# Kernel tuning notes

Measured on AMD Instinct MI355X. Metric: run time of the kernel, lower is better.

## Reference

```python
import jax, jax.numpy as jnp
import numpy as np

B, S, E, H, D = 2, 2048, 1024, 16, 64  # batch, seq(=max_seq_len), embed_dim, heads, atten_dim


def setup_inputs() -> dict:
    key = jax.random.key(0)
    ks = jax.random.split(key, 9)
    s = 0.02
    return {
        "x": jax.random.normal(ks[0], (B, S, E), jnp.float32),
        "Wq": jax.random.normal(ks[1], (H, E, D), jnp.float32) * s,
        "Wk": jax.random.normal(ks[2], (H, E, D), jnp.float32) * s,
        "Wv": jax.random.normal(ks[3], (H, E, D), jnp.float32) * s,
        "bq": jax.random.normal(ks[4], (H, D), jnp.float32) * s,
        "bk": jax.random.normal(ks[5], (H, D), jnp.float32) * s,
        "bv": jax.random.normal(ks[6], (H, D), jnp.float32) * s,
        "Wp": jax.random.normal(ks[7], (H * D, E), jnp.float32) * s,
        "bp": jax.random.normal(ks[8], (E,), jnp.float32) * s,
    }


def reference(x, Wq, Wk, Wv, bq, bk, bv, Wp, bp):
    scale = jnp.sqrt(jnp.float32(D))
    # per-head projections, all heads at once: [B,H,S,D]
    q = jnp.einsum("bse,hed->bhsd", x, Wq) + bq[:, None, :]
    k = jnp.einsum("bse,hed->bhsd", x, Wk) + bk[:, None, :]
    v = jnp.einsum("bse,hed->bhsd", x, Wv) + bv[:, None, :]
    # causal scores [B,H,S,S], additive -inf mask above diagonal (as in the buffer)
    score = jnp.einsum("bhsd,bhtd->bhst", q, k) / scale
    mask = jnp.triu(jnp.full((S, S), -jnp.inf, jnp.float32), k=1)
    score = score + mask
    probs = jax.nn.softmax(score, axis=-1)
    attn = jnp.einsum("bhst,bhtd->bhsd", probs, v)
    # concat heads -> [B,S,H*D], then projection + ReLU
    concat = attn.transpose(0, 2, 1, 3).reshape(B, S, H * D)
    out = jax.nn.relu(concat @ Wp + bp)
    return out
```

## Files before the change

### kernel.cpp

```cpp
#include <hip/hip_runtime.h>

#define S_LEN 2048
#define E_DIM 1024
#define H_NUM 16
#define D_DIM 64

typedef unsigned short u16;
using bf16x8 = __attribute__((ext_vector_type(8))) short;
using f32x4  = __attribute__((ext_vector_type(4))) float;

#define MFMA16(A, B, C) __builtin_amdgcn_mfma_f32_16x16x32_bf16(A, B, C, 0, 0, 0)
#define QSCALE 0.18033688011112042f

__device__ __forceinline__ u16 f2bf(float f) {
    unsigned u = __float_as_uint(f);
    u += 0x7fffu + ((u >> 16) & 1u);
    return (u16)(u >> 16);
}
__device__ __forceinline__ f32x4 fzero4() { f32x4 z; z[0]=0.f; z[1]=0.f; z[2]=0.f; z[3]=0.f; return z; }

__device__ __forceinline__ unsigned cvtpk(float a, float b) {
    unsigned r;
    asm("v_cvt_pk_bf16_f32 %0, %1, %2" : "=v"(r) : "v"(a), "v"(b));
    return r;
}
__device__ __forceinline__ float fexp2(float x) {
#if __has_builtin(__builtin_amdgcn_exp2f)
    return __builtin_amdgcn_exp2f(x);
#else
    float r; asm("v_exp_f32 %0, %1" : "=v"(r) : "v"(x)); return r;
#endif
}
__device__ __forceinline__ float frcp(float x) {
#if __has_builtin(__builtin_amdgcn_rcpf)
    return __builtin_amdgcn_rcpf(x);
#else
    float r; asm("v_rcp_f32 %0, %1" : "=v"(r) : "v"(x)); return r;
#endif
}

__device__ __forceinline__ void gll16(const u16* g, u16* l) {
    __builtin_amdgcn_global_load_lds(
        (const __attribute__((address_space(1))) void*)g,
        (__attribute__((address_space(3))) void*)l, 16, 0, 0);
}

__device__ __forceinline__ void stage64(const u16* __restrict__ g, int gstride,
                                        u16* l, int wave, int lane) {
    #pragma unroll
    for (int i = 0; i < 2; i++) {
        const int r  = wave * 16 + i * 8 + (lane >> 3);
        const int sl = (lane & 7) ^ (r & 7);
        gll16(g + (size_t)r * gstride + sl * 8, l + (wave * 16 + i * 8) * 64);
    }
}
__device__ __forceinline__ bf16x8 ldswz(const u16* t, int rr, int hh, int quad) {
    const int sl = ((hh << 2) + quad) ^ (rr & 7);
    return *(const bf16x8*)(t + rr * 64 + sl * 8);
}

__global__ __launch_bounds__(256) void cvt_bf16(const float* __restrict__ in, u16* __restrict__ outp, int n) {
    int i4 = (blockIdx.x * 256 + threadIdx.x) * 4;
    if (i4 < n) {
        float4 f = *(const float4*)(in + i4);
        unsigned lo = (unsigned)f2bf(f.x) | ((unsigned)f2bf(f.y) << 16);
        unsigned hi = (unsigned)f2bf(f.z) | ((unsigned)f2bf(f.w) << 16);
        uint2 p; p.x = lo; p.y = hi;
        *(uint2*)(outp + i4) = p;
    }
}

__device__ __forceinline__ void cvt_t_tile(const float* __restrict__ bin, u16* __restrict__ bout,
                                           int R, int C, int r0, int c0) {
    __shared__ float t[64][65];
    const int tid = threadIdx.x;
    const int lr = tid >> 2, lc = (tid & 3) * 16;

    const float* src = bin + (size_t)(r0 + lr) * C + c0 + lc;
    #pragma unroll
    for (int j = 0; j < 4; j++) {
        float4 f = *(const float4*)(src + j * 4);
        t[lr][lc + j * 4 + 0] = f.x; t[lr][lc + j * 4 + 1] = f.y;
        t[lr][lc + j * 4 + 2] = f.z; t[lr][lc + j * 4 + 3] = f.w;
    }
    __syncthreads();

    u16* dst = bout + (size_t)(c0 + lr) * R + r0 + lc;
    u16 vals[16];
    #pragma unroll
    for (int i = 0; i < 16; i++) vals[i] = f2bf(t[lc + i][lr]);
    uint4 pa, pb;
    pa.x = vals[0] | (vals[1] << 16);  pa.y = vals[2] | (vals[3] << 16);
    pa.z = vals[4] | (vals[5] << 16);  pa.w = vals[6] | (vals[7] << 16);
    pb.x = vals[8] | (vals[9] << 16);  pb.y = vals[10] | (vals[11] << 16);
    pb.z = vals[12] | (vals[13] << 16); pb.w = vals[14] | (vals[15] << 16);
    *(uint4*)dst = pa;
    *(uint4*)(dst + 8) = pb;
}

__global__ __launch_bounds__(256) void cvt_bf16_t(const float* __restrict__ in, u16* __restrict__ outp,
                                                  int R, int C) {
    const float* bin = in + (size_t)blockIdx.z * R * C;
    u16* bout = outp + (size_t)blockIdx.z * R * C;
    cvt_t_tile(bin, bout, R, C, blockIdx.y * 64, blockIdx.x * 64);
}

__global__ __launch_bounds__(256) void cvt_w3_t(
    const float* __restrict__ Wq, const float* __restrict__ Wk, const float* __restrict__ Wv,
    u16* __restrict__ wqt, u16* __restrict__ wkt, u16* __restrict__ wvt) {
    const int which = blockIdx.z >> 4, bh = blockIdx.z & 15;
    const float* in = (which == 0) ? Wq : (which == 1) ? Wk : Wv;
    u16* outp = (which == 0) ? wqt : (which == 1) ? wkt : wvt;
    const float* bin = in + (size_t)bh * E_DIM * D_DIM;
    u16* bout = outp + (size_t)bh * E_DIM * D_DIM;
    cvt_t_tile(bin, bout, E_DIM, D_DIM, blockIdx.y * 64, 0);
}

__global__ __launch_bounds__(256) void qkv_gemm(
    const u16* __restrict__ xb, const u16* __restrict__ wcat,
    const float* __restrict__ bq, const float* __restrict__ bk, const float* __restrict__ bv,
    u16* __restrict__ oq, u16* __restrict__ okk, u16* __restrict__ ov)
{
    const int m0 = blockIdx.x * 128;
    const int n0 = blockIdx.y * 128;

    __shared__ u16 As[128 * 64];
    __shared__ u16 Bs[128 * 64];

    const int tid  = threadIdx.x;
    const int wave = tid >> 6, lane = tid & 63, quad = lane >> 4, l16 = lane & 15;
    const int mh = wave >> 1, nh = wave & 1;

    f32x4 acc[4][4];
    #pragma unroll
    for (int j = 0; j < 4; j++)
        #pragma unroll
        for (int mi = 0; mi < 4; mi++) acc[j][mi] = fzero4();

    for (int k0 = 0; k0 < E_DIM; k0 += 64) {
        __syncthreads();
        #pragma unroll
        for (int i = 0; i < 4; i++) {
            const int r  = wave * 32 + i * 8 + (lane >> 3);
            const int sl = (lane & 7) ^ (r & 7);
            gll16(xb   + (size_t)(m0 + r) * E_DIM + k0 + sl * 8, &As[(wave * 32 + i * 8) * 64]);
            gll16(wcat + (size_t)(n0 + r) * E_DIM + k0 + sl * 8, &Bs[(wave * 32 + i * 8) * 64]);
        }
        __syncthreads();

        #pragma unroll
        for (int kq = 0; kq < 2; kq++) {
            bf16x8 af[4];
            #pragma unroll
            for (int mi = 0; mi < 4; mi++) {
                const int rr = mh * 64 + mi * 16 + l16;
                af[mi] = *(const bf16x8*)(&As[rr * 64 + (((kq << 2) + quad) ^ (rr & 7)) * 8]);
            }
            #pragma unroll
            for (int j = 0; j < 4; j++) {
                const int rr = nh * 64 + j * 16 + l16;
                bf16x8 bfv = *(const bf16x8*)(&Bs[rr * 64 + (((kq << 2) + quad) ^ (rr & 7)) * 8]);
                #pragma unroll
                for (int mi = 0; mi < 4; mi++)
                    acc[j][mi] = MFMA16(af[mi], bfv, acc[j][mi]);
            }
        }
    }

    const int t = n0 >> 10;
    if (t < 2) {
        const float scl = (t == 0) ? QSCALE : 1.0f;
        const float* bias = (t == 0) ? bq : bk;
        u16* dst = (t == 0) ? oq : okk;
        #pragma unroll
        for (int j = 0; j < 4; j++) {
            const int n = n0 + nh * 64 + j * 16 + l16;
            const int h = (n >> 6) & 15, d = n & 63;
            float bia = bias[h * D_DIM + d];
            #pragma unroll
            for (int mi = 0; mi < 4; mi++) {
                #pragma unroll
                for (int r = 0; r < 4; r++) {
                    int m = m0 + mh * 64 + mi * 16 + quad * 4 + r;
                    int b = m >> 11, s = m & 2047;
                    dst[((size_t)(b * H_NUM + h) * S_LEN + s) * D_DIM + d] =
                        f2bf((acc[j][mi][r] + bia) * scl);
                }
            }
        }
    } else {
        const int b  = m0 >> 11, s0 = m0 & 2047;
        const int h0 = (n0 >> 6) & 15;
        u16* Tb0 = As;
        u16* Tb1 = Bs;
        #pragma unroll
        for (int pass = 0; pass < 2; ++pass) {
            __syncthreads();
            if (mh == pass) {
                u16* Tb = nh ? Tb1 : Tb0;
                #pragma unroll
                for (int j = 0; j < 4; j++) {
                    const int n = n0 + nh * 64 + j * 16 + l16;
                    const int d = n & 63, hh = (n >> 6) & 15;
                    const float bia = bv[hh * D_DIM + d];
                    const int nl = j * 16 + l16;
                    #pragma unroll
                    for (int mi = 0; mi < 4; mi++) {
                        uint2 pk;
                        pk.x = cvtpk(acc[j][mi][0] + bia, acc[j][mi][1] + bia);
                        pk.y = cvtpk(acc[j][mi][2] + bia, acc[j][mi][3] + bia);
                        *(uint2*)(&Tb[nl * 72 + mi * 16 + quad * 4]) = pk;
                    }
                }
            }
            __syncthreads();
            #pragma unroll
            for (int g = 0; g < 4; ++g) {
                const int rowi = g * 32 + (tid >> 3);
                const int ml = (tid & 7) * 8;
                const u16* srcp = (rowi < 64 ? Tb0 : Tb1) + (rowi & 63) * 72 + ml;
                const int hh = h0 + (rowi >> 6), d = rowi & 63;
                u16* dstp = ov + ((size_t)(b * H_NUM + hh) * D_DIM + d) * S_LEN
                               + s0 + pass * 64 + ml;
                *(uint4*)dstp = *(const uint4*)srcp;
            }
        }
    }
}

__global__ __launch_bounds__(256, 2) void attn_fwd(
    const u16* __restrict__ q, const u16* __restrict__ k, const u16* __restrict__ vt,
    u16* __restrict__ concat)
{
    const int bid  = blockIdx.x;
    const int halfg = bid >> 8;
    const int pi   = (bid & 255) >> 5;
    const int p    = halfg ? (15 - pi) : pi;
    const int g    = bid & 31;
    const int h    = g & 15;
    const int bb   = g >> 4;
    const int qa = p, qb = 31 - p;

    const size_t headoff = (size_t)(bb * H_NUM + h) * S_LEN * D_DIM;
    const u16* qh  = q  + headoff;
    const u16* kh  = k  + headoff;
    const u16* vth = vt + headoff;

    __shared__ u16 QaL[64 * 64];
    __shared__ u16 QbL[64 * 64];
    __shared__ u16 Ks[2][64 * 64];
    __shared__ u16 Vts[2][64 * 64];
    __shared__ u16 Psa[4][16 * 72];
    __shared__ u16 Psb[4][16 * 72];

    const int tid  = threadIdx.x;
    const int wave = tid >> 6, lane = tid & 63, quad = lane >> 4, l16 = lane & 15;

    stage64(qh + (size_t)qa * 64 * D_DIM, D_DIM, QaL,    wave, lane);
    stage64(qh + (size_t)qb * 64 * D_DIM, D_DIM, QbL,    wave, lane);
    stage64(kh,                           D_DIM, Ks[0],  wave, lane);
    stage64(vth,                          S_LEN, Vts[0], wave, lane);
    __syncthreads();

    bf16x8 bqa0 = ldswz(QaL, wave * 16 + l16, 0, quad);
    bf16x8 bqa1 = ldswz(QaL, wave * 16 + l16, 1, quad);
    bf16x8 bqb0 = ldswz(QbL, wave * 16 + l16, 0, quad);
    bf16x8 bqb1 = ldswz(QbL, wave * 16 + l16, 1, quad);

    f32x4 oa[4], ob[4];
    #pragma unroll
    for (int nt = 0; nt < 4; nt++) { oa[nt] = fzero4(); ob[nt] = fzero4(); }
    float la = 0.f, lb = 0.f;

    const int qga = qa * 64 + wave * 16 + l16;
    const int qgb = qb * 64 + wave * 16 + l16;

    u16* pwa = &Psa[wave][0];
    u16* pwb = &Psb[wave][0];

    for (int kt = 0; kt <= qb; kt++) {
        __syncthreads();
        if (kt < qb) {
            stage64(kh + (size_t)(kt + 1) * 64 * D_DIM, D_DIM, Ks[(kt + 1) & 1],  wave, lane);
            stage64(vth + (kt + 1) * 64,                S_LEN, Vts[(kt + 1) & 1], wave, lane);
        }
        const u16* Kc = Ks[kt & 1];
        const u16* Vc = Vts[kt & 1];
        const bool both = (kt <= qa);

        f32x4 stb[4], sta[4];
        #pragma unroll
        for (int nt = 0; nt < 4; nt++) {
            const int rr = nt * 16 + l16;
            bf16x8 ak0 = ldswz(Kc, rr, 0, quad);
            bf16x8 ak1 = ldswz(Kc, rr, 1, quad);
            stb[nt] = MFMA16(ak0, bqb0, fzero4());
            stb[nt] = MFMA16(ak1, bqb1, stb[nt]);
            if (both) {
                sta[nt] = MFMA16(ak0, bqa0, fzero4());
                sta[nt] = MFMA16(ak1, bqa1, sta[nt]);
            }
        }

        bf16x8 bv0[4], bv1[4];
        #pragma unroll
        for (int nt = 0; nt < 4; nt++) {
            bv0[nt] = ldswz(Vc, nt * 16 + l16, 0, quad);
            bv1[nt] = ldswz(Vc, nt * 16 + l16, 1, quad);
        }

        #pragma unroll
        for (int nt = 0; nt < 4; nt++) {
            float pe[4];
            if (kt == qb) {
                #pragma unroll
                for (int r = 0; r < 4; r++) {
                    int kkg = kt * 64 + nt * 16 + quad * 4 + r;
                    pe[r] = (kkg > qgb) ? 0.f : fexp2(stb[nt][r]);
                }
            } else {
                #pragma unroll
                for (int r = 0; r < 4; r++) pe[r] = fexp2(stb[nt][r]);
            }
            lb += (pe[0] + pe[1]) + (pe[2] + pe[3]);
            uint2 pk;
            pk.x = cvtpk(pe[0], pe[1]);
            pk.y = cvtpk(pe[2], pe[3]);
            *(uint2*)(&pwb[l16 * 72 + nt * 16 + quad * 4]) = pk;
        }
        if (both) {
            #pragma unroll
            for (int nt = 0; nt < 4; nt++) {
                float pe[4];
                if (kt == qa) {
                    #pragma unroll
                    for (int r = 0; r < 4; r++) {
                        int kkg = kt * 64 + nt * 16 + quad * 4 + r;
                        pe[r] = (kkg > qga) ? 0.f : fexp2(sta[nt][r]);
                    }
                } else {
                    #pragma unroll
                    for (int r = 0; r < 4; r++) pe[r] = fexp2(sta[nt][r]);
                }
                la += (pe[0] + pe[1]) + (pe[2] + pe[3]);
                uint2 pk;
                pk.x = cvtpk(pe[0], pe[1]);
                pk.y = cvtpk(pe[2], pe[3]);
                *(uint2*)(&pwa[l16 * 72 + nt * 16 + quad * 4]) = pk;
            }
        }

        {
            bf16x8 ap0 = *(const bf16x8*)(&pwb[l16 * 72 + quad * 8]);
            bf16x8 ap1 = *(const bf16x8*)(&pwb[l16 * 72 + 32 + quad * 8]);
            #pragma unroll
            for (int nt = 0; nt < 4; nt++) {
                ob[nt] = MFMA16(ap0, bv0[nt], ob[nt]);
                ob[nt] = MFMA16(ap1, bv1[nt], ob[nt]);
            }
        }
        if (both) {
            bf16x8 ap0 = *(const bf16x8*)(&pwa[l16 * 72 + quad * 8]);
            bf16x8 ap1 = *(const bf16x8*)(&pwa[l16 * 72 + 32 + quad * 8]);
            #pragma unroll
            for (int nt = 0; nt < 4; nt++) {
                oa[nt] = MFMA16(ap0, bv0[nt], oa[nt]);
                oa[nt] = MFMA16(ap1, bv1[nt], oa[nt]);
            }
        }
    }

    lb += __shfl_xor(lb, 16); lb += __shfl_xor(lb, 32);
    la += __shfl_xor(la, 16); la += __shfl_xor(la, 32);

    #pragma unroll
    for (int r = 0; r < 4; r++) {
        const int srcl = quad * 4 + r;
        float lbi = frcp(__shfl(lb, srcl));
        float lai = frcp(__shfl(la, srcl));
        int sqa = qa * 64 + wave * 16 + quad * 4 + r;
        int sqb = qb * 64 + wave * 16 + quad * 4 + r;
        #pragma unroll
        for (int nt = 0; nt < 4; nt++) {
            concat[((size_t)(bb * S_LEN + sqa)) * E_DIM + h * D_DIM + nt * 16 + l16] =
                f2bf(oa[nt][r] * lai);
            concat[((size_t)(bb * S_LEN + sqb)) * E_DIM + h * D_DIM + nt * 16 + l16] =
                f2bf(ob[nt][r] * lbi);
        }
    }
}

__global__ __launch_bounds__(256) void out_proj(
    const u16* __restrict__ concat, const u16* __restrict__ wpt,
    const float* __restrict__ bp, float* __restrict__ out)
{
    const int m0 = blockIdx.x * 128;
    const int n0 = blockIdx.y * 128;

    __shared__ u16 As[128 * 40];
    __shared__ u16 Bs[128 * 40];

    const int tid  = threadIdx.x;
    const int wave = tid >> 6, lane = tid & 63, quad = lane >> 4, l16 = lane & 15;
    const int mh = wave >> 1, nh = wave & 1;

    const int arow = tid >> 1, acol = (tid & 1) * 16;

    const u16* aptr = concat + (size_t)(m0 + arow) * E_DIM + acol;
    const u16* bptr = wpt + (size_t)(n0 + arow) * E_DIM + acol;

    f32x4 acc[4][4];
    #pragma unroll
    for (int j = 0; j < 4; j++)
        #pragma unroll
        for (int mi = 0; mi < 4; mi++) acc[j][mi] = fzero4();

    uint4 pA0, pA1, pB0, pB1;
    pA0 = *(const uint4*)(aptr);     pA1 = *(const uint4*)(aptr + 8);
    pB0 = *(const uint4*)(bptr);     pB1 = *(const uint4*)(bptr + 8);

    for (int k0 = 0; k0 < E_DIM; k0 += 32) {
        __syncthreads();
        *(uint4*)(&As[arow * 40 + acol    ]) = pA0;
        *(uint4*)(&As[arow * 40 + acol + 8]) = pA1;
        *(uint4*)(&Bs[arow * 40 + acol    ]) = pB0;
        *(uint4*)(&Bs[arow * 40 + acol + 8]) = pB1;
        __syncthreads();

        if (k0 + 32 < E_DIM) {
            pA0 = *(const uint4*)(aptr + k0 + 32);  pA1 = *(const uint4*)(aptr + k0 + 40);
            pB0 = *(const uint4*)(bptr + k0 + 32);  pB1 = *(const uint4*)(bptr + k0 + 40);
        }

        bf16x8 af[4];
        #pragma unroll
        for (int mi = 0; mi < 4; mi++)
            af[mi] = *(const bf16x8*)(&As[(mh * 64 + mi * 16 + l16) * 40 + quad * 8]);
        #pragma unroll
        for (int j = 0; j < 4; j++) {
            bf16x8 bfv = *(const bf16x8*)(&Bs[(nh * 64 + j * 16 + l16) * 40 + quad * 8]);
            #pragma unroll
            for (int mi = 0; mi < 4; mi++)
                acc[j][mi] = MFMA16(af[mi], bfv, acc[j][mi]);
        }
    }

    #pragma unroll
    for (int j = 0; j < 4; j++) {
        int n = n0 + nh * 64 + j * 16 + l16;
        float bia = bp[n];
        #pragma unroll
        for (int mi = 0; mi < 4; mi++) {
            #pragma unroll
            for (int r = 0; r < 4; r++) {
                int m = m0 + mh * 64 + mi * 16 + quad * 4 + r;
                out[(size_t)m * E_DIM + n] = fmaxf(acc[j][mi][r] + bia, 0.f);
            }
        }
    }
}

extern "C" void kernel_launch(void* const* d_in, const int* in_sizes, int n_in,
                              void* d_out, int out_size, void* d_ws, size_t ws_size,
                              hipStream_t stream)
{
    (void)in_sizes; (void)n_in; (void)out_size; (void)ws_size;
    const float* x  = (const float*)d_in[0];
    const float* Wq = (const float*)d_in[1];
    const float* Wk = (const float*)d_in[2];
    const float* Wv = (const float*)d_in[3];
    const float* bq = (const float*)d_in[4];
    const float* bk = (const float*)d_in[5];
    const float* bv = (const float*)d_in[6];
    const float* Wp = (const float*)d_in[7];
    const float* bp = (const float*)d_in[8];
    float* out = (float*)d_out;

    const size_t QKV_ELEMS = (size_t)2 * H_NUM * S_LEN * D_DIM;
    const size_t W_ELEMS   = (size_t)H_NUM * E_DIM * D_DIM;

    u16* q   = (u16*)d_ws;
    u16* k   = q   + QKV_ELEMS;
    u16* v   = k   + QKV_ELEMS;
    u16* cc  = v   + QKV_ELEMS;
    u16* xb  = cc  + QKV_ELEMS;
    u16* wqt = xb  + QKV_ELEMS;
    u16* wkt = wqt + W_ELEMS;
    u16* wvt = wkt + W_ELEMS;
    u16* wpt = wvt + W_ELEMS;

    cvt_bf16<<<dim3(4096), 256, 0, stream>>>(x, xb, (int)QKV_ELEMS);
    cvt_w3_t<<<dim3(1, 16, 48), 256, 0, stream>>>(Wq, Wk, Wv, wqt, wkt, wvt);
    cvt_bf16_t<<<dim3(16, 16, 1), 256, 0, stream>>>(Wp, wpt, H_NUM * D_DIM, E_DIM);

    qkv_gemm<<<dim3(32, 24), 256, 0, stream>>>(xb, wqt, bq, bk, bv, q, k, v);
    attn_fwd<<<dim3(512), 256, 0, stream>>>(q, k, v, cc);
    out_proj<<<dim3(32, 8), 256, 0, stream>>>(cc, wpt, bp, out);
}
```

Before: 191.7 us.

## Merge conversion kernels, swizzle GEMM block order, and retile out_proj with LDS DMA

New measurement: 182.9 us. 4.6% less time.

```diff
diff --git a/kernel.cpp b/kernel.cpp
--- a/kernel.cpp
+++ b/kernel.cpp
@@ -57,17 +57,6 @@
 __device__ __forceinline__ bf16x8 ldswz(const u16* t, int rr, int hh, int quad) {
     const int sl = ((hh << 2) + quad) ^ (rr & 7);
     return *(const bf16x8*)(t + rr * 64 + sl * 8);
-}
-
-__global__ __launch_bounds__(256) void cvt_bf16(const float* __restrict__ in, u16* __restrict__ outp, int n) {
-    int i4 = (blockIdx.x * 256 + threadIdx.x) * 4;
-    if (i4 < n) {
-        float4 f = *(const float4*)(in + i4);
-        unsigned lo = (unsigned)f2bf(f.x) | ((unsigned)f2bf(f.y) << 16);
-        unsigned hi = (unsigned)f2bf(f.z) | ((unsigned)f2bf(f.w) << 16);
-        uint2 p; p.x = lo; p.y = hi;
-        *(uint2*)(outp + i4) = p;
-    }
 }
 
 __device__ __forceinline__ void cvt_t_tile(const float* __restrict__ bin, u16* __restrict__ bout,
@@ -98,22 +87,35 @@
     *(uint4*)(dst + 8) = pb;
 }
 
-__global__ __launch_bounds__(256) void cvt_bf16_t(const float* __restrict__ in, u16* __restrict__ outp,
-                                                  int R, int C) {
-    const float* bin = in + (size_t)blockIdx.z * R * C;
-    u16* bout = outp + (size_t)blockIdx.z * R * C;
-    cvt_t_tile(bin, bout, R, C, blockIdx.y * 64, blockIdx.x * 64);
-}
-
-__global__ __launch_bounds__(256) void cvt_w3_t(
+__global__ __launch_bounds__(256) void cvt_all(
+    const float* __restrict__ x, u16* __restrict__ xb, int n,
     const float* __restrict__ Wq, const float* __restrict__ Wk, const float* __restrict__ Wv,
-    u16* __restrict__ wqt, u16* __restrict__ wkt, u16* __restrict__ wvt) {
-    const int which = blockIdx.z >> 4, bh = blockIdx.z & 15;
-    const float* in = (which == 0) ? Wq : (which == 1) ? Wk : Wv;
-    u16* outp = (which == 0) ? wqt : (which == 1) ? wkt : wvt;
-    const float* bin = in + (size_t)bh * E_DIM * D_DIM;
-    u16* bout = outp + (size_t)bh * E_DIM * D_DIM;
-    cvt_t_tile(bin, bout, E_DIM, D_DIM, blockIdx.y * 64, 0);
+    u16* __restrict__ wqt, u16* __restrict__ wkt, u16* __restrict__ wvt,
+    const float* __restrict__ Wp, u16* __restrict__ wpt)
+{
+    const int bid = blockIdx.x;
+    if (bid < 4096) {
+        int i4 = (bid * 256 + threadIdx.x) * 4;
+        if (i4 < n) {
+            float4 f = *(const float4*)(x + i4);
+            unsigned lo = (unsigned)f2bf(f.x) | ((unsigned)f2bf(f.y) << 16);
+            unsigned hi = (unsigned)f2bf(f.z) | ((unsigned)f2bf(f.w) << 16);
+            uint2 p; p.x = lo; p.y = hi;
+            *(uint2*)(xb + i4) = p;
+        }
+    } else if (bid < 4096 + 768) {
+        const int t  = bid - 4096;
+        const int z  = t >> 4;
+        const int ry = t & 15;
+        const int which = z >> 4, bh = z & 15;
+        const float* in = (which == 0) ? Wq : (which == 1) ? Wk : Wv;
+        u16* outp = (which == 0) ? wqt : (which == 1) ? wkt : wvt;
+        cvt_t_tile(in + (size_t)bh * E_DIM * D_DIM, outp + (size_t)bh * E_DIM * D_DIM,
+                   E_DIM, D_DIM, ry * 64, 0);
+    } else {
+        const int t = bid - (4096 + 768);
+        cvt_t_tile(Wp, wpt, H_NUM * D_DIM, E_DIM, (t >> 4) * 64, (t & 15) * 64);
+    }
 }
 
 __global__ __launch_bounds__(256) void qkv_gemm(
@@ -121,8 +123,10 @@
     const float* __restrict__ bq, const float* __restrict__ bk, const float* __restrict__ bv,
     u16* __restrict__ oq, u16* __restrict__ okk, u16* __restrict__ ov)
 {
-    const int m0 = blockIdx.x * 128;
-    const int n0 = blockIdx.y * 128;
+    const int bid = blockIdx.x;
+    const int sw  = (bid & 7) * 96 + (bid >> 3);
+    const int m0  = (sw & 31) * 128;
+    const int n0  = (sw >> 5) * 128;
 
     __shared__ u16 As[128 * 64];
     __shared__ u16 Bs[128 * 64];
@@ -289,6 +293,7 @@
         const bool both = (kt <= qa);
 
         f32x4 stb[4], sta[4];
+        __builtin_amdgcn_s_setprio(1);
         #pragma unroll
         for (int nt = 0; nt < 4; nt++) {
             const int rr = nt * 16 + l16;
@@ -301,6 +306,7 @@
                 sta[nt] = MFMA16(ak1, bqa1, sta[nt]);
             }
         }
+        __builtin_amdgcn_s_setprio(0);
 
         bf16x8 bv0[4], bv1[4];
         #pragma unroll
@@ -353,20 +359,24 @@
         {
             bf16x8 ap0 = *(const bf16x8*)(&pwb[l16 * 72 + quad * 8]);
             bf16x8 ap1 = *(const bf16x8*)(&pwb[l16 * 72 + 32 + quad * 8]);
+            __builtin_amdgcn_s_setprio(1);
             #pragma unroll
             for (int nt = 0; nt < 4; nt++) {
                 ob[nt] = MFMA16(ap0, bv0[nt], ob[nt]);
                 ob[nt] = MFMA16(ap1, bv1[nt], ob[nt]);
             }
+            __builtin_amdgcn_s_setprio(0);
         }
         if (both) {
             bf16x8 ap0 = *(const bf16x8*)(&pwa[l16 * 72 + quad * 8]);
             bf16x8 ap1 = *(const bf16x8*)(&pwa[l16 * 72 + 32 + quad * 8]);
+            __builtin_amdgcn_s_setprio(1);
             #pragma unroll
             for (int nt = 0; nt < 4; nt++) {
                 oa[nt] = MFMA16(ap0, bv0[nt], oa[nt]);
                 oa[nt] = MFMA16(ap1, bv1[nt], oa[nt]);
             }
+            __builtin_amdgcn_s_setprio(0);
         }
     }
 
@@ -390,58 +400,61 @@
     }
 }
 
-__global__ __launch_bounds__(256) void out_proj(
+__global__ __launch_bounds__(256, 2) void out_proj(
     const u16* __restrict__ concat, const u16* __restrict__ wpt,
     const float* __restrict__ bp, float* __restrict__ out)
 {
-    const int m0 = blockIdx.x * 128;
-    const int n0 = blockIdx.y * 128;
-
-    __shared__ u16 As[128 * 40];
-    __shared__ u16 Bs[128 * 40];
+    const int bid = blockIdx.x;
+    const int mt  = (bid & 7) * 8 + ((bid >> 3) & 7);
+    const int nt0 = bid >> 6;
+    const int m0 = mt * 64;
+    const int n0 = nt0 * 128;
+
+    __shared__ u16 As[2][64 * 64];
+    __shared__ u16 Bs[2][128 * 64];
 
     const int tid  = threadIdx.x;
     const int wave = tid >> 6, lane = tid & 63, quad = lane >> 4, l16 = lane & 15;
     const int mh = wave >> 1, nh = wave & 1;
 
-    const int arow = tid >> 1, acol = (tid & 1) * 16;
-
-    const u16* aptr = concat + (size_t)(m0 + arow) * E_DIM + acol;
-    const u16* bptr = wpt + (size_t)(n0 + arow) * E_DIM + acol;
-
-    f32x4 acc[4][4];
+    f32x4 acc[4][2];
     #pragma unroll
     for (int j = 0; j < 4; j++)
         #pragma unroll
-        for (int mi = 0; mi < 4; mi++) acc[j][mi] = fzero4();
-
-    uint4 pA0, pA1, pB0, pB1;
-    pA0 = *(const uint4*)(aptr);     pA1 = *(const uint4*)(aptr + 8);
-    pB0 = *(const uint4*)(bptr);     pB1 = *(const uint4*)(bptr + 8);
-
-    for (int k0 = 0; k0 < E_DIM; k0 += 32) {
+        for (int mi = 0; mi < 2; mi++) acc[j][mi] = fzero4();
+
+    stage64(concat + (size_t)m0 * E_DIM, E_DIM, As[0], wave, lane);
+    stage64(wpt + (size_t)n0 * E_DIM,        E_DIM, Bs[0],           wave, lane);
+    stage64(wpt + (size_t)(n0 + 64) * E_DIM, E_DIM, Bs[0] + 64 * 64, wave, lane);
+
+    for (int kt = 0; kt < 16; kt++) {
         __syncthreads();
-        *(uint4*)(&As[arow * 40 + acol    ]) = pA0;
-        *(uint4*)(&As[arow * 40 + acol + 8]) = pA1;
-        *(uint4*)(&Bs[arow * 40 + acol    ]) = pB0;
-        *(uint4*)(&Bs[arow * 40 + acol + 8]) = pB1;
-        __syncthreads();
-
-        if (k0 + 32 < E_DIM) {
-            pA0 = *(const uint4*)(aptr + k0 + 32);  pA1 = *(const uint4*)(aptr + k0 + 40);
-            pB0 = *(const uint4*)(bptr + k0 + 32);  pB1 = *(const uint4*)(bptr + k0 + 40);
-        }
-
-        bf16x8 af[4];
-        #pragma unroll
-        for (int mi = 0; mi < 4; mi++)
-            af[mi] = *(const bf16x8*)(&As[(mh * 64 + mi * 16 + l16) * 40 + quad * 8]);
-        #pragma unroll
-        for (int j = 0; j < 4; j++) {
-            bf16x8 bfv = *(const bf16x8*)(&Bs[(nh * 64 + j * 16 + l16) * 40 + quad * 8]);
-            #pragma unroll
-            for (int mi = 0; mi < 4; mi++)
-                acc[j][mi] = MFMA16(af[mi], bfv, acc[j][mi]);
+        if (kt < 15) {
+            const int k0 = (kt + 1) * 64;
+            u16* an = As[(kt + 1) & 1];
+            u16* bn = Bs[(kt + 1) & 1];
+            stage64(concat + (size_t)m0 * E_DIM + k0, E_DIM, an, wave, lane);
+            stage64(wpt + (size_t)n0 * E_DIM + k0,        E_DIM, bn,           wave, lane);
+            stage64(wpt + (size_t)(n0 + 64) * E_DIM + k0, E_DIM, bn + 64 * 64, wave, lane);
+        }
+        const u16* Ac = As[kt & 1];
+        const u16* Bc = Bs[kt & 1];
+
+        #pragma unroll
+        for (int kq = 0; kq < 2; kq++) {
+            bf16x8 af[2];
+            #pragma unroll
+            for (int mi = 0; mi < 2; mi++)
+                af[mi] = ldswz(Ac, mh * 32 + mi * 16 + l16, kq, quad);
+            __builtin_amdgcn_s_setprio(1);
+            #pragma unroll
+            for (int j = 0; j < 4; j++) {
+                bf16x8 bfv = ldswz(Bc, nh * 64 + j * 16 + l16, kq, quad);
+                #pragma unroll
+                for (int mi = 0; mi < 2; mi++)
+                    acc[j][mi] = MFMA16(af[mi], bfv, acc[j][mi]);
+            }
+            __builtin_amdgcn_s_setprio(0);
         }
     }
 
@@ -450,10 +463,10 @@
         int n = n0 + nh * 64 + j * 16 + l16;
         float bia = bp[n];
         #pragma unroll
-        for (int mi = 0; mi < 4; mi++) {
+        for (int mi = 0; mi < 2; mi++) {
             #pragma unroll
             for (int r = 0; r < 4; r++) {
-                int m = m0 + mh * 64 + mi * 16 + quad * 4 + r;
+                int m = m0 + mh * 32 + mi * 16 + quad * 4 + r;
                 out[(size_t)m * E_DIM + n] = fmaxf(acc[j][mi][r] + bia, 0.f);
             }
         }
@@ -489,11 +502,10 @@
     u16* wvt = wkt + W_ELEMS;
     u16* wpt = wvt + W_ELEMS;
 
-    cvt_bf16<<<dim3(4096), 256, 0, stream>>>(x, xb, (int)QKV_ELEMS);
-    cvt_w3_t<<<dim3(1, 16, 48), 256, 0, stream>>>(Wq, Wk, Wv, wqt, wkt, wvt);
-    cvt_bf16_t<<<dim3(16, 16, 1), 256, 0, stream>>>(Wp, wpt, H_NUM * D_DIM, E_DIM);
-
-    qkv_gemm<<<dim3(32, 24), 256, 0, stream>>>(xb, wqt, bq, bk, bv, q, k, v);
+    cvt_all<<<dim3(4096 + 768 + 256), 256, 0, stream>>>(
+        x, xb, (int)QKV_ELEMS, Wq, Wk, Wv, wqt, wkt, wvt, Wp, wpt);
+
+    qkv_gemm<<<dim3(768), 256, 0, stream>>>(xb, wqt, bq, bk, bv, q, k, v);
     attn_fwd<<<dim3(512), 256, 0, stream>>>(q, k, v, cc);
-    out_proj<<<dim3(32, 8), 256, 0, stream>>>(cc, wpt, bp, out);
-}
+    out_proj<<<dim3(512), 256, 0, stream>>>(cc, wpt, bp, out);
+}
```
